# Kernel optimization log

Measured on AMD Instinct MI355X. Metric: run time of the kernel, lower is better.

The kernel has to match this reference:

```python
import jax, jax.numpy as jnp
import numpy as np

N_NODES = 50000
N_EDGES = 800000


def _graph_conv(src, dst, x, W, b, act=None):
    """DGL GraphConv with norm='both', edge_weight=None.
    out = D_in^{-1/2} * segsum_dst( (x * D_out^{-1/2})[src] @ W ) + b
    (W applied before aggregation: same math, cheaper when out_dim < in_dim).
    """
    n = x.shape[0]
    ones = jnp.ones(src.shape[0], dtype=x.dtype)
    deg_out = jax.ops.segment_sum(ones, src, num_segments=n)  # out-degree of src nodes
    deg_in = jax.ops.segment_sum(ones, dst, num_segments=n)   # in-degree of dst nodes
    norm_src = jax.lax.rsqrt(jnp.maximum(deg_out, 1.0))
    norm_dst = jax.lax.rsqrt(jnp.maximum(deg_in, 1.0))
    h = (x * norm_src[:, None]) @ W                 # [N, out]
    agg = jax.ops.segment_sum(h[src], dst, num_segments=n)  # gather+scatter-add [N, out]
    out = agg * norm_dst[:, None] + b
    return act(out) if act is not None else out


def setup_inputs() -> dict:
    key = jax.random.key(0)
    ks = jax.random.split(key, 6)
    x = jax.random.normal(ks[0], (N_NODES, 256), dtype=jnp.float32)
    W1 = jax.random.normal(ks[1], (256, 128), dtype=jnp.float32) * (1.0 / np.sqrt(256))
    b1 = jnp.zeros((128,), dtype=jnp.float32)
    W2 = jax.random.normal(ks[2], (128, 40), dtype=jnp.float32) * (1.0 / np.sqrt(128))
    b2 = jnp.zeros((40,), dtype=jnp.float32)
    edge_src = jax.random.randint(ks[3], (N_EDGES,), 0, N_NODES, dtype=jnp.int32)
    edge_dst = jax.random.randint(ks[4], (N_EDGES,), 0, N_NODES, dtype=jnp.int32)
    return {"x": x, "W1": W1, "b1": b1, "W2": W2, "b2": b2,
            "edge_src": edge_src, "edge_dst": edge_dst}


def reference(x, W1, b1, W2, b2, edge_src, edge_dst):
    h = _graph_conv(edge_src, edge_dst, x, W1, b1, act=jax.nn.relu)
    # dropout is identity in eval mode
    out = _graph_conv(edge_src, edge_dst, h, W2, b2, act=None)
    return out
```

## Files before the change

kernel.cpp:

```cpp
#include <hip/hip_runtime.h>
#include <cstdint>
#include <cstddef>

typedef unsigned int u32;
typedef unsigned short u16;


__device__ __forceinline__ u16 f2bf(float f) {
    u32 u = __builtin_bit_cast(u32, f);
    u = u + 0x7FFFu + ((u >> 16) & 1u);
    return (u16)(u >> 16);
}
__device__ __forceinline__ float bf2f_lo(u32 p) { return __builtin_bit_cast(float, p << 16); }
__device__ __forceinline__ float bf2f_hi(u32 p) { return __builtin_bit_cast(float, p & 0xFFFF0000u); }
__device__ __forceinline__ float bf2f(u16 v) { return __builtin_bit_cast(float, (u32)v << 16); }

__global__ __launch_bounds__(256) void k_zero(u32* __restrict__ a, int n2) {
    int i = blockIdx.x * 256 + threadIdx.x;
    if (i < n2) a[i] = 0u;
}

__global__ __launch_bounds__(256, 4) void k_gemm1_fill(
    const float* __restrict__ x, const float* __restrict__ W, u16* __restrict__ hb,
    int n, int gblocks,
    const int* __restrict__ src, const int* __restrict__ dst,
    u32* __restrict__ cnt_out, u32* __restrict__ cnt_in,
    int* __restrict__ bucket, int cap, int e) {
    if ((int)blockIdx.x >= gblocks) {
        int fb = blockIdx.x - gblocks;
        int base = (fb * 256 + (int)threadIdx.x) * 4;
        if (base >= e) return;
        int s[4], d[4];
        u32 pos[4];
        int nv;
        if (base + 4 <= e) {
            int4 s4 = *(const int4*)&src[base];
            int4 d4 = *(const int4*)&dst[base];
            s[0] = s4.x; s[1] = s4.y; s[2] = s4.z; s[3] = s4.w;
            d[0] = d4.x; d[1] = d4.y; d[2] = d4.z; d[3] = d4.w;
            nv = 4;
        } else {
            nv = e - base;
            for (int j = 0; j < nv; j++) { s[j] = src[base + j]; d[j] = dst[base + j]; }
        }
#pragma unroll
        for (int j = 0; j < 4; j++) if (j < nv) atomicAdd(&cnt_out[s[j]], 1u);
#pragma unroll
        for (int j = 0; j < 4; j++) if (j < nv) pos[j] = atomicAdd(&cnt_in[d[j]], 1u);
#pragma unroll
        for (int j = 0; j < 4; j++) if (j < nv && (int)pos[j] < cap) bucket[(size_t)d[j] * cap + pos[j]] = s[j];
        return;
    }
    __shared__ float xs[64][32];
    __shared__ float ws[32][128];
    const int t = threadIdx.x;
    const int tcol = t & 31;
    const int trow = t >> 5;
    const int row0 = blockIdx.x * 64;

    float acc[8][4];
#pragma unroll
    for (int i = 0; i < 8; i++)
#pragma unroll
        for (int j = 0; j < 4; j++) acc[i][j] = 0.f;

    for (int k0 = 0; k0 < 256; k0 += 32) {
#pragma unroll
        for (int l = 0; l < 2; l++) {
            int f = t + l * 256;
            int r = f >> 3, c4 = f & 7;
            int gr = row0 + r;
            float4 v = make_float4(0.f, 0.f, 0.f, 0.f);
            if (gr < n) v = *(const float4*)&x[(size_t)gr * 256 + k0 + c4 * 4];
            *(float4*)&xs[r][c4 * 4] = v;
        }
#pragma unroll
        for (int l = 0; l < 4; l++) {
            int f = t + l * 256;
            int r = f >> 5, c4 = f & 31;
            *(float4*)&ws[r][c4 * 4] = *(const float4*)&W[(size_t)(k0 + r) * 128 + c4 * 4];
        }
        __syncthreads();
#pragma unroll
        for (int kk = 0; kk < 32; kk += 4) {
            float4 xv[8];
#pragma unroll
            for (int i = 0; i < 8; i++) xv[i] = *(const float4*)&xs[trow * 8 + i][kk];
            float4 wv[4];
#pragma unroll
            for (int j = 0; j < 4; j++) wv[j] = *(const float4*)&ws[kk + j][tcol * 4];
#pragma unroll
            for (int i = 0; i < 8; i++) {
                acc[i][0] = fmaf(xv[i].x, wv[0].x, acc[i][0]);
                acc[i][1] = fmaf(xv[i].x, wv[0].y, acc[i][1]);
                acc[i][2] = fmaf(xv[i].x, wv[0].z, acc[i][2]);
                acc[i][3] = fmaf(xv[i].x, wv[0].w, acc[i][3]);
                acc[i][0] = fmaf(xv[i].y, wv[1].x, acc[i][0]);
                acc[i][1] = fmaf(xv[i].y, wv[1].y, acc[i][1]);
                acc[i][2] = fmaf(xv[i].y, wv[1].z, acc[i][2]);
                acc[i][3] = fmaf(xv[i].y, wv[1].w, acc[i][3]);
                acc[i][0] = fmaf(xv[i].z, wv[2].x, acc[i][0]);
                acc[i][1] = fmaf(xv[i].z, wv[2].y, acc[i][1]);
                acc[i][2] = fmaf(xv[i].z, wv[2].z, acc[i][2]);
                acc[i][3] = fmaf(xv[i].z, wv[2].w, acc[i][3]);
                acc[i][0] = fmaf(xv[i].w, wv[3].x, acc[i][0]);
                acc[i][1] = fmaf(xv[i].w, wv[3].y, acc[i][1]);
                acc[i][2] = fmaf(xv[i].w, wv[3].z, acc[i][2]);
                acc[i][3] = fmaf(xv[i].w, wv[3].w, acc[i][3]);
            }
        }
        __syncthreads();
    }
#pragma unroll
    for (int i = 0; i < 8; i++) {
        int gr = row0 + trow * 8 + i;
        if (gr < n) {
            u32 p0 = (u32)f2bf(acc[i][0]) | ((u32)f2bf(acc[i][1]) << 16);
            u32 p1 = (u32)f2bf(acc[i][2]) | ((u32)f2bf(acc[i][3]) << 16);
            uint2 o = make_uint2(p0, p1);
            *(uint2*)&hb[(size_t)gr * 128 + tcol * 4] = o;
        }
    }
}

__global__ __launch_bounds__(256) void k_agg1_gemm2(
    const u16* __restrict__ hb, const u32* __restrict__ cnt_out, const u32* __restrict__ cnt_in,
    const int* __restrict__ bucket, int cap,
    const float* __restrict__ b1, const float* __restrict__ W2,
    u16* __restrict__ h2b, int n) {
    __shared__ u32 xsp[64][66];
    __shared__ float ws[32][40];
    const int t = threadIdx.x;
    const int wid = t >> 6, lane = t & 63;
    const int half = lane >> 5;
    const int hl = lane & 31;
    const int row0 = blockIdx.x * 64;
    const int c = hl * 4;

    for (int pi = 0; pi < 8; ++pi) {
        int r = wid * 16 + half * 8 + pi;
        int node = row0 + r;
        u32 cin = 0, cout = 0;
        if (node < n) { cin = cnt_in[node]; cout = cnt_out[node]; }
        int cnt = (int)cin; if (cnt > cap) cnt = cap;
        int s = node * cap, epos = s + cnt;
        float a0 = 0.f, a1 = 0.f, a2 = 0.f, a3 = 0.f;
        int i = s;
        for (; i + 8 <= epos; i += 8) {
            int idx[8];
#pragma unroll
            for (int j = 0; j < 8; j++) idx[j] = bucket[i + j];
            u32 co[8];
#pragma unroll
            for (int j = 0; j < 8; j++) co[j] = cnt_out[idx[j]];
            uint2 pv[8];
#pragma unroll
            for (int j = 0; j < 8; j++) pv[j] = *(const uint2*)&hb[(size_t)idx[j] * 128 + c];
#pragma unroll
            for (int j = 0; j < 8; j++) {
                float ns = rsqrtf(fmaxf((float)co[j], 1.0f));
                a0 = fmaf(ns, bf2f_lo(pv[j].x), a0);
                a1 = fmaf(ns, bf2f_hi(pv[j].x), a1);
                a2 = fmaf(ns, bf2f_lo(pv[j].y), a2);
                a3 = fmaf(ns, bf2f_hi(pv[j].y), a3);
            }
        }
        if (i + 4 <= epos) {
            int i0 = bucket[i], i1 = bucket[i + 1], i2 = bucket[i + 2], i3 = bucket[i + 3];
            u32 c0 = cnt_out[i0], c1 = cnt_out[i1], c2 = cnt_out[i2], c3 = cnt_out[i3];
            uint2 p0 = *(const uint2*)&hb[(size_t)i0 * 128 + c];
            uint2 p1 = *(const uint2*)&hb[(size_t)i1 * 128 + c];
            uint2 p2 = *(const uint2*)&hb[(size_t)i2 * 128 + c];
            uint2 p3 = *(const uint2*)&hb[(size_t)i3 * 128 + c];
            float n0 = rsqrtf(fmaxf((float)c0, 1.f)), n1 = rsqrtf(fmaxf((float)c1, 1.f));
            float n2 = rsqrtf(fmaxf((float)c2, 1.f)), n3 = rsqrtf(fmaxf((float)c3, 1.f));
            a0 = fmaf(n0, bf2f_lo(p0.x), fmaf(n1, bf2f_lo(p1.x), fmaf(n2, bf2f_lo(p2.x), fmaf(n3, bf2f_lo(p3.x), a0))));
            a1 = fmaf(n0, bf2f_hi(p0.x), fmaf(n1, bf2f_hi(p1.x), fmaf(n2, bf2f_hi(p2.x), fmaf(n3, bf2f_hi(p3.x), a1))));
            a2 = fmaf(n0, bf2f_lo(p0.y), fmaf(n1, bf2f_lo(p1.y), fmaf(n2, bf2f_lo(p2.y), fmaf(n3, bf2f_lo(p3.y), a2))));
            a3 = fmaf(n0, bf2f_hi(p0.y), fmaf(n1, bf2f_hi(p1.y), fmaf(n2, bf2f_hi(p2.y), fmaf(n3, bf2f_hi(p3.y), a3))));
            i += 4;
        }
        if (i + 2 <= epos) {
            int i0 = bucket[i], i1 = bucket[i + 1];
            u32 c0 = cnt_out[i0], c1 = cnt_out[i1];
            uint2 p0 = *(const uint2*)&hb[(size_t)i0 * 128 + c];
            uint2 p1 = *(const uint2*)&hb[(size_t)i1 * 128 + c];
            float n0 = rsqrtf(fmaxf((float)c0, 1.f)), n1 = rsqrtf(fmaxf((float)c1, 1.f));
            a0 = fmaf(n0, bf2f_lo(p0.x), fmaf(n1, bf2f_lo(p1.x), a0));
            a1 = fmaf(n0, bf2f_hi(p0.x), fmaf(n1, bf2f_hi(p1.x), a1));
            a2 = fmaf(n0, bf2f_lo(p0.y), fmaf(n1, bf2f_lo(p1.y), a2));
            a3 = fmaf(n0, bf2f_hi(p0.y), fmaf(n1, bf2f_hi(p1.y), a3));
            i += 2;
        }
        if (i < epos) {
            int i0 = bucket[i];
            float n0 = rsqrtf(fmaxf((float)cnt_out[i0], 1.f));
            uint2 p0 = *(const uint2*)&hb[(size_t)i0 * 128 + c];
            a0 = fmaf(n0, bf2f_lo(p0.x), a0);
            a1 = fmaf(n0, bf2f_hi(p0.x), a1);
            a2 = fmaf(n0, bf2f_lo(p0.y), a2);
            a3 = fmaf(n0, bf2f_hi(p0.y), a3);
        }
        if (node < n) {
            float nd = rsqrtf(fmaxf((float)cin, 1.0f));
            float nsn = rsqrtf(fmaxf((float)cout, 1.0f));
            float o0 = fmaxf(fmaf(a0, nd, b1[c]), 0.f) * nsn;
            float o1 = fmaxf(fmaf(a1, nd, b1[c + 1]), 0.f) * nsn;
            float o2 = fmaxf(fmaf(a2, nd, b1[c + 2]), 0.f) * nsn;
            float o3 = fmaxf(fmaf(a3, nd, b1[c + 3]), 0.f) * nsn;
            xsp[r][hl * 2] = (u32)f2bf(o0) | ((u32)f2bf(o1) << 16);
            xsp[r][hl * 2 + 1] = (u32)f2bf(o2) | ((u32)f2bf(o3) << 16);
        } else {
            xsp[r][hl * 2] = 0u;
            xsp[r][hl * 2 + 1] = 0u;
        }
    }
    __syncthreads();

    const int tcol = t & 7;
    const int trow = t >> 3;
    float acc[2][5];
#pragma unroll
    for (int i = 0; i < 2; i++)
#pragma unroll
        for (int j = 0; j < 5; j++) acc[i][j] = 0.f;

    for (int k0 = 0; k0 < 128; k0 += 32) {
        for (int l = t; l < 1280; l += 256) {
            int rr = l / 40, cc = l % 40;
            ws[rr][cc] = W2[(size_t)(k0 + rr) * 40 + cc];
        }
        __syncthreads();
#pragma unroll 4
        for (int kk = 0; kk < 32; kk += 2) {
            float w0a = ws[kk][tcol * 5 + 0], w0b = ws[kk + 1][tcol * 5 + 0];
            float w1a = ws[kk][tcol * 5 + 1], w1b = ws[kk + 1][tcol * 5 + 1];
            float w2a = ws[kk][tcol * 5 + 2], w2b = ws[kk + 1][tcol * 5 + 2];
            float w3a = ws[kk][tcol * 5 + 3], w3b = ws[kk + 1][tcol * 5 + 3];
            float w4a = ws[kk][tcol * 5 + 4], w4b = ws[kk + 1][tcol * 5 + 4];
#pragma unroll
            for (int i = 0; i < 2; i++) {
                u32 pv = xsp[trow * 2 + i][(k0 + kk) >> 1];
                float xa = bf2f_lo(pv);
                float xb = bf2f_hi(pv);
                acc[i][0] = fmaf(xa, w0a, fmaf(xb, w0b, acc[i][0]));
                acc[i][1] = fmaf(xa, w1a, fmaf(xb, w1b, acc[i][1]));
                acc[i][2] = fmaf(xa, w2a, fmaf(xb, w2b, acc[i][2]));
                acc[i][3] = fmaf(xa, w3a, fmaf(xb, w3b, acc[i][3]));
                acc[i][4] = fmaf(xa, w4a, fmaf(xb, w4b, acc[i][4]));
            }
        }
        __syncthreads();
    }
#pragma unroll
    for (int i = 0; i < 2; i++) {
        int gr = row0 + trow * 2 + i;
        if (gr < n) {
#pragma unroll
            for (int j = 0; j < 5; j++) h2b[(size_t)gr * 40 + tcol * 5 + j] = f2bf(acc[i][j]);
        }
    }
}

__global__ __launch_bounds__(256) void k_agg2(const u16* __restrict__ h2b, const u32* __restrict__ cnt_in,
                                              const int* __restrict__ bucket, int cap,
                                              const float* __restrict__ b2, float* __restrict__ out, int n) {
    int node = (blockIdx.x * 256 + threadIdx.x) >> 6;
    int lane = threadIdx.x & 63;
    if (node >= n) return;
    u32 cin = cnt_in[node];
    int cnt = (int)cin; if (cnt > cap) cnt = cap;
    int s = node * cap, epos = s + cnt;
    if (lane >= 40) return;
    float acc = 0.f;
    int i = s;
    for (; i + 8 <= epos; i += 8) {
        int idx[8];
#pragma unroll
        for (int j = 0; j < 8; j++) idx[j] = bucket[i + j];
        u16 v[8];
#pragma unroll
        for (int j = 0; j < 8; j++) v[j] = h2b[(size_t)idx[j] * 40 + lane];
#pragma unroll
        for (int j = 0; j < 8; j++) acc += bf2f(v[j]);
    }
    if (i + 4 <= epos) {
        int i0 = bucket[i], i1 = bucket[i + 1], i2 = bucket[i + 2], i3 = bucket[i + 3];
        u16 v0 = h2b[(size_t)i0 * 40 + lane];
        u16 v1 = h2b[(size_t)i1 * 40 + lane];
        u16 v2 = h2b[(size_t)i2 * 40 + lane];
        u16 v3 = h2b[(size_t)i3 * 40 + lane];
        acc += bf2f(v0) + bf2f(v1) + bf2f(v2) + bf2f(v3);
        i += 4;
    }
    if (i + 2 <= epos) {
        int i0 = bucket[i], i1 = bucket[i + 1];
        acc += bf2f(h2b[(size_t)i0 * 40 + lane]) + bf2f(h2b[(size_t)i1 * 40 + lane]);
        i += 2;
    }
    if (i < epos) acc += bf2f(h2b[(size_t)bucket[i] * 40 + lane]);
    float nd = rsqrtf(fmaxf((float)cin, 1.0f));
    out[(size_t)node * 40 + lane] = fmaf(acc, nd, b2[lane]);
}

static inline char* align_up(char* p, size_t a) {
    return (char*)(((uintptr_t)p + (a - 1)) & ~(uintptr_t)(a - 1));
}

extern "C" void kernel_launch(void* const* d_in, const int* in_sizes, int n_in,
                              void* d_out, int out_size, void* d_ws, size_t ws_size,
                              hipStream_t stream) {
    const float* x  = (const float*)d_in[0];
    const float* W1 = (const float*)d_in[1];
    const float* b1 = (const float*)d_in[2];
    const float* W2 = (const float*)d_in[3];
    const float* b2 = (const float*)d_in[4];
    const int* esrc = (const int*)d_in[5];
    const int* edst = (const int*)d_in[6];
    float* out = (float*)d_out;

    const int n = in_sizes[0] / 256;
    const int e = in_sizes[5];

    char* p = (char*)d_ws;
    u32* cnt_out = (u32*)p;            p = align_up(p + (size_t)n * 4, 256);
    u32* cnt_in  = (u32*)p;            p = align_up(p + (size_t)n * 4, 256);
    u16* hb      = (u16*)p;            p = align_up(p + (size_t)n * 128 * 2, 256);
    u16* h2b     = (u16*)p;            p = align_up(p + (size_t)n * 40 * 2, 256);
    size_t used = (size_t)(p - (char*)d_ws);
    int cap = 64;
    if (used + (size_t)n * 64 * 4 > ws_size) cap = 48;
    if (used + (size_t)n * (size_t)cap * 4 > ws_size) cap = 32;
    int* bucket = (int*)p;

    const int gblocks = (n + 63) / 64;
    const int fblocks = (e / 4 + 255) / 256;
    const int nb256 = (n + 255) / 256;

    k_zero<<<nb256, 256, 0, stream>>>(cnt_out, n);
    k_zero<<<nb256, 256, 0, stream>>>(cnt_in, n);
    k_gemm1_fill<<<gblocks + fblocks, 256, 0, stream>>>(x, W1, hb, n, gblocks,
                                                        esrc, edst, cnt_out, cnt_in, bucket, cap, e);
    k_agg1_gemm2<<<(n + 63) / 64, 256, 0, stream>>>(hb, cnt_out, cnt_in, bucket, cap, b1, W2, h2b, n);
    k_agg2<<<(n + 3) / 4, 256, 0, stream>>>(h2b, cnt_in, bucket, cap, b2, out, n);
}
```

Before: 170.9 us.

## Pre-scale layer-1 features by source norm in a separate pass; one edge per thread in fill

Adds a k_scale kernel that multiplies each row of the bf16 hidden features by its source-degree rsqrt after the GEMM. The aggregation then sums the gathered rows directly, without the per-edge dependent cnt_out load and rsqrt. The edge-fill path also goes back to one edge per thread with scalar loads. The cost is an extra kernel launch, an extra read and write of hb, and a second bf16 rounding of the features.

```diff
diff --git a/kernel.cpp b/kernel.cpp
--- a/kernel.cpp
+++ b/kernel.cpp
@@ -27,28 +27,12 @@
     u32* __restrict__ cnt_out, u32* __restrict__ cnt_in,
     int* __restrict__ bucket, int cap, int e) {
     if ((int)blockIdx.x >= gblocks) {
-        int fb = blockIdx.x - gblocks;
-        int base = (fb * 256 + (int)threadIdx.x) * 4;
-        if (base >= e) return;
-        int s[4], d[4];
-        u32 pos[4];
-        int nv;
-        if (base + 4 <= e) {
-            int4 s4 = *(const int4*)&src[base];
-            int4 d4 = *(const int4*)&dst[base];
-            s[0] = s4.x; s[1] = s4.y; s[2] = s4.z; s[3] = s4.w;
-            d[0] = d4.x; d[1] = d4.y; d[2] = d4.z; d[3] = d4.w;
-            nv = 4;
-        } else {
-            nv = e - base;
-            for (int j = 0; j < nv; j++) { s[j] = src[base + j]; d[j] = dst[base + j]; }
-        }
-#pragma unroll
-        for (int j = 0; j < 4; j++) if (j < nv) atomicAdd(&cnt_out[s[j]], 1u);
-#pragma unroll
-        for (int j = 0; j < 4; j++) if (j < nv) pos[j] = atomicAdd(&cnt_in[d[j]], 1u);
-#pragma unroll
-        for (int j = 0; j < 4; j++) if (j < nv && (int)pos[j] < cap) bucket[(size_t)d[j] * cap + pos[j]] = s[j];
+        int i = (blockIdx.x - gblocks) * 256 + (int)threadIdx.x;
+        if (i >= e) return;
+        int s = src[i], d = dst[i];
+        atomicAdd(&cnt_out[s], 1u);
+        u32 pos = atomicAdd(&cnt_in[d], 1u);
+        if ((int)pos < cap) bucket[(size_t)d * cap + pos] = s;
         return;
     }
     __shared__ float xs[64][32];
@@ -123,6 +107,21 @@
     }
 }
 
+__global__ __launch_bounds__(256) void k_scale(u16* __restrict__ hb, const u32* __restrict__ cnt_out, int n) {
+    int gid = blockIdx.x * 256 + threadIdx.x;
+    int total = n * 16;
+    if (gid >= total) return;
+    int row = gid >> 4;
+    float ns = rsqrtf(fmaxf((float)cnt_out[row], 1.0f));
+    uint4* p = (uint4*)&hb[(size_t)row * 128 + (gid & 15) * 8];
+    uint4 v = *p;
+    u32 r0 = (u32)f2bf(bf2f_lo(v.x) * ns) | ((u32)f2bf(bf2f_hi(v.x) * ns) << 16);
+    u32 r1 = (u32)f2bf(bf2f_lo(v.y) * ns) | ((u32)f2bf(bf2f_hi(v.y) * ns) << 16);
+    u32 r2 = (u32)f2bf(bf2f_lo(v.z) * ns) | ((u32)f2bf(bf2f_hi(v.z) * ns) << 16);
+    u32 r3 = (u32)f2bf(bf2f_lo(v.w) * ns) | ((u32)f2bf(bf2f_hi(v.w) * ns) << 16);
+    *p = make_uint4(r0, r1, r2, r3);
+}
+
 __global__ __launch_bounds__(256) void k_agg1_gemm2(
     const u16* __restrict__ hb, const u32* __restrict__ cnt_out, const u32* __restrict__ cnt_in,
     const int* __restrict__ bucket, int cap,
@@ -150,56 +149,46 @@
             int idx[8];
 #pragma unroll
             for (int j = 0; j < 8; j++) idx[j] = bucket[i + j];
-            u32 co[8];
-#pragma unroll
-            for (int j = 0; j < 8; j++) co[j] = cnt_out[idx[j]];
             uint2 pv[8];
 #pragma unroll
             for (int j = 0; j < 8; j++) pv[j] = *(const uint2*)&hb[(size_t)idx[j] * 128 + c];
 #pragma unroll
             for (int j = 0; j < 8; j++) {
-                float ns = rsqrtf(fmaxf((float)co[j], 1.0f));
-                a0 = fmaf(ns, bf2f_lo(pv[j].x), a0);
-                a1 = fmaf(ns, bf2f_hi(pv[j].x), a1);
-                a2 = fmaf(ns, bf2f_lo(pv[j].y), a2);
-                a3 = fmaf(ns, bf2f_hi(pv[j].y), a3);
+                a0 += bf2f_lo(pv[j].x);
+                a1 += bf2f_hi(pv[j].x);
+                a2 += bf2f_lo(pv[j].y);
+                a3 += bf2f_hi(pv[j].y);
             }
         }
         if (i + 4 <= epos) {
             int i0 = bucket[i], i1 = bucket[i + 1], i2 = bucket[i + 2], i3 = bucket[i + 3];
-            u32 c0 = cnt_out[i0], c1 = cnt_out[i1], c2 = cnt_out[i2], c3 = cnt_out[i3];
             uint2 p0 = *(const uint2*)&hb[(size_t)i0 * 128 + c];
             uint2 p1 = *(const uint2*)&hb[(size_t)i1 * 128 + c];
             uint2 p2 = *(const uint2*)&hb[(size_t)i2 * 128 + c];
             uint2 p3 = *(const uint2*)&hb[(size_t)i3 * 128 + c];
-            float n0 = rsqrtf(fmaxf((float)c0, 1.f)), n1 = rsqrtf(fmaxf((float)c1, 1.f));
-            float n2 = rsqrtf(fmaxf((float)c2, 1.f)), n3 = rsqrtf(fmaxf((float)c3, 1.f));
-            a0 = fmaf(n0, bf2f_lo(p0.x), fmaf(n1, bf2f_lo(p1.x), fmaf(n2, bf2f_lo(p2.x), fmaf(n3, bf2f_lo(p3.x), a0))));
-            a1 = fmaf(n0, bf2f_hi(p0.x), fmaf(n1, bf2f_hi(p1.x), fmaf(n2, bf2f_hi(p2.x), fmaf(n3, bf2f_hi(p3.x), a1))));
-            a2 = fmaf(n0, bf2f_lo(p0.y), fmaf(n1, bf2f_lo(p1.y), fmaf(n2, bf2f_lo(p2.y), fmaf(n3, bf2f_lo(p3.y), a2))));
-            a3 = fmaf(n0, bf2f_hi(p0.y), fmaf(n1, bf2f_hi(p1.y), fmaf(n2, bf2f_hi(p2.y), fmaf(n3, bf2f_hi(p3.y), a3))));
+            a0 += bf2f_lo(p0.x) + bf2f_lo(p1.x) + bf2f_lo(p2.x) + bf2f_lo(p3.x);
+            a1 += bf2f_hi(p0.x) + bf2f_hi(p1.x) + bf2f_hi(p2.x) + bf2f_hi(p3.x);
+            a2 += bf2f_lo(p0.y) + bf2f_lo(p1.y) + bf2f_lo(p2.y) + bf2f_lo(p3.y);
+            a3 += bf2f_hi(p0.y) + bf2f_hi(p1.y) + bf2f_hi(p2.y) + bf2f_hi(p3.y);
             i += 4;
         }
         if (i + 2 <= epos) {
             int i0 = bucket[i], i1 = bucket[i + 1];
-            u32 c0 = cnt_out[i0], c1 = cnt_out[i1];
             uint2 p0 = *(const uint2*)&hb[(size_t)i0 * 128 + c];
             uint2 p1 = *(const uint2*)&hb[(size_t)i1 * 128 + c];
-            float n0 = rsqrtf(fmaxf((float)c0, 1.f)), n1 = rsqrtf(fmaxf((float)c1, 1.f));
-            a0 = fmaf(n0, bf2f_lo(p0.x), fmaf(n1, bf2f_lo(p1.x), a0));
-            a1 = fmaf(n0, bf2f_hi(p0.x), fmaf(n1, bf2f_hi(p1.x), a1));
-            a2 = fmaf(n0, bf2f_lo(p0.y), fmaf(n1, bf2f_lo(p1.y), a2));
-            a3 = fmaf(n0, bf2f_hi(p0.y), fmaf(n1, bf2f_hi(p1.y), a3));
+            a0 += bf2f_lo(p0.x) + bf2f_lo(p1.x);
+            a1 += bf2f_hi(p0.x) + bf2f_hi(p1.x);
+            a2 += bf2f_lo(p0.y) + bf2f_lo(p1.y);
+            a3 += bf2f_hi(p0.y) + bf2f_hi(p1.y);
             i += 2;
         }
         if (i < epos) {
             int i0 = bucket[i];
-            float n0 = rsqrtf(fmaxf((float)cnt_out[i0], 1.f));
             uint2 p0 = *(const uint2*)&hb[(size_t)i0 * 128 + c];
-            a0 = fmaf(n0, bf2f_lo(p0.x), a0);
-            a1 = fmaf(n0, bf2f_hi(p0.x), a1);
-            a2 = fmaf(n0, bf2f_lo(p0.y), a2);
-            a3 = fmaf(n0, bf2f_hi(p0.y), a3);
+            a0 += bf2f_lo(p0.x);
+            a1 += bf2f_hi(p0.x);
+            a2 += bf2f_lo(p0.y);
+            a3 += bf2f_hi(p0.y);
         }
         if (node < n) {
             float nd = rsqrtf(fmaxf((float)cin, 1.0f));
@@ -334,13 +323,14 @@
     int* bucket = (int*)p;
 
     const int gblocks = (n + 63) / 64;
-    const int fblocks = (e / 4 + 255) / 256;
+    const int fblocks = (e + 255) / 256;
     const int nb256 = (n + 255) / 256;
 
     k_zero<<<nb256, 256, 0, stream>>>(cnt_out, n);
     k_zero<<<nb256, 256, 0, stream>>>(cnt_in, n);
     k_gemm1_fill<<<gblocks + fblocks, 256, 0, stream>>>(x, W1, hb, n, gblocks,
                                                         esrc, edst, cnt_out, cnt_in, bucket, cap, e);
+    k_scale<<<(n * 16 + 255) / 256, 256, 0, stream>>>(hb, cnt_out, n);
     k_agg1_gemm2<<<(n + 63) / 64, 256, 0, stream>>>(hb, cnt_out, cnt_in, bucket, cap, b1, W2, h2b, n);
     k_agg2<<<(n + 3) / 4, 256, 0, stream>>>(h2b, cnt_in, bucket, cap, b2, out, n);
 }
```

Result: no change. 168.0 us (-1.7%).
